# Optimization experiments

Measured on AMD Instinct MI355X. Metric: run time of the kernel, lower is better.

The kernel has to match this reference:

```python
import jax, jax.numpy as jnp
import numpy as np
import math

V, D = 100000, 128
B, L = 4096, 200
INIT_MU = 0.1
INIT_RHO = math.log(math.exp(0.01 ** 0.5) - 1.0)  # softplus^-1(sqrt(init_sigma2))


def setup_inputs() -> dict:
    key = jax.random.key(0)
    k_mu, k_eps, k_x = jax.random.split(key, 3)
    W_mu = jax.random.uniform(k_mu, (V, D), jnp.float32, -INIT_MU, INIT_MU)
    W_rho = jnp.full((V, D), INIT_RHO, dtype=jnp.float32)
    eps = jax.random.normal(k_eps, (V, D), jnp.float32)
    x = jax.random.randint(k_x, (B, L), 0, V)
    return {"x": x, "W_mu": W_mu, "W_rho": W_rho, "eps": eps}


def reference(x, W_mu, W_rho, eps):
    # sigma = softplus(rho); sampled table = mu + sigma * clip(eps, -10, 10)
    W_sigma = jnp.log1p(jnp.exp(W_rho))
    sampled = W_mu + W_sigma * jnp.clip(eps, -10.0, 10.0)  # [V, D]
    return jnp.take(sampled, x, axis=0)  # [B, L, D]
```

## Files before the change

kernel.cpp:

```cpp
#include <hip/hip_runtime.h>
#include <hip/hip_bf16.h>

typedef float f32x4 __attribute__((ext_vector_type(4)));

#define D4 32

__device__ __forceinline__ float softplus_f(float r) {
    return (r > 20.0f) ? r : log1pf(__expf(r));
}
__device__ __forceinline__ float clip10(float e) {
    return fminf(fmaxf(e, -10.0f), 10.0f);
}

__global__ __launch_bounds__(256) void sample_table_kernel(
    const f32x4* __restrict__ mu,
    const f32x4* __restrict__ rho,
    const f32x4* __restrict__ eps,
    f32x4* __restrict__ sampled,
    long n4)
{
    long i = (long)blockIdx.x * blockDim.x + threadIdx.x;
    if (i >= n4) return;
    f32x4 m = __builtin_nontemporal_load(&mu[i]);
    f32x4 r = __builtin_nontemporal_load(&rho[i]);
    f32x4 e = __builtin_nontemporal_load(&eps[i]);
    f32x4 o;
    o.x = m.x + softplus_f(r.x) * clip10(e.x);
    o.y = m.y + softplus_f(r.y) * clip10(e.y);
    o.z = m.z + softplus_f(r.z) * clip10(e.z);
    o.w = m.w + softplus_f(r.w) * clip10(e.w);
    sampled[i] = o;
}

__global__ __launch_bounds__(256) void gather_kernel(
    const int* __restrict__ x,
    const f32x4* __restrict__ sampled,
    f32x4* __restrict__ out,
    int n_rows)
{
    int tid  = blockIdx.x * blockDim.x + threadIdx.x;
    int row  = tid >> 5;
    int lane = tid & 31;
    if (row >= n_rows) return;
    int v = x[row];
    f32x4 val = sampled[(long)v * D4 + lane];
    __builtin_nontemporal_store(val, &out[(long)row * D4 + lane]);
}

__global__ __launch_bounds__(256) void fused_kernel(
    const int* __restrict__ x,
    const f32x4* __restrict__ mu,
    const f32x4* __restrict__ rho,
    const f32x4* __restrict__ eps,
    f32x4* __restrict__ out,
    int n_rows)
{
    int tid  = blockIdx.x * blockDim.x + threadIdx.x;
    int row  = tid >> 5;
    int lane = tid & 31;
    if (row >= n_rows) return;
    long src = (long)x[row] * D4 + lane;
    f32x4 m = mu[src], r = rho[src], e = eps[src];
    f32x4 o;
    o.x = m.x + softplus_f(r.x) * clip10(e.x);
    o.y = m.y + softplus_f(r.y) * clip10(e.y);
    o.z = m.z + softplus_f(r.z) * clip10(e.z);
    o.w = m.w + softplus_f(r.w) * clip10(e.w);
    out[(long)row * D4 + lane] = o;
}

extern "C" void kernel_launch(void* const* d_in, const int* in_sizes, int n_in,
                              void* d_out, int out_size, void* d_ws, size_t ws_size,
                              hipStream_t stream)
{
    const int*   x   = (const int*)  d_in[0];
    const f32x4* mu  = (const f32x4*)d_in[1];
    const f32x4* rho = (const f32x4*)d_in[2];
    const f32x4* eps = (const f32x4*)d_in[3];
    f32x4* out = (f32x4*)d_out;

    int  n_rows      = in_sizes[0];
    long table_elems = (long)in_sizes[1];
    size_t table_bytes = (size_t)table_elems * sizeof(float);
    const int block = 256;

    if (ws_size >= table_bytes) {
        f32x4* sampled = (f32x4*)d_ws;
        long n4 = table_elems / 4;

        int grid1 = (int)((n4 + block - 1) / block);
        sample_table_kernel<<<grid1, block, 0, stream>>>(mu, rho, eps, sampled, n4);

        long threads2 = (long)n_rows * 32;
        int grid2 = (int)((threads2 + block - 1) / block);
        gather_kernel<<<grid2, block, 0, stream>>>(x, sampled, out, n_rows);
    } else {
        long threads = (long)n_rows * 32;
        int grid = (int)((threads + block - 1) / block);
        fused_kernel<<<grid, block, 0, stream>>>(x, mu, rho, eps, out, n_rows);
    }
}
```

Before: 160.7 us.

## Store sampled embedding table in bf16 and gather two rows per thread

The sampled table is written to the workspace as bf16 instead of fp32, halving its footprint and the bytes written by the sampling pass and read by the gather. The gather kernel expands bf16 back to fp32 and handles two output rows per thread slot. This reduces memory traffic and cache pressure but introduces bf16 rounding error in the output values.

```diff
diff --git a/kernel.cpp b/kernel.cpp
--- a/kernel.cpp
+++ b/kernel.cpp
@@ -2,6 +2,10 @@
 #include <hip/hip_bf16.h>
 
 typedef float f32x4 __attribute__((ext_vector_type(4)));
+typedef unsigned short u16;
+typedef unsigned int   u32;
+typedef u16 u16x4 __attribute__((ext_vector_type(4)));
+typedef u16 u16x8 __attribute__((ext_vector_type(8)));
 
 #define D4 32
 
@@ -11,40 +15,82 @@
 __device__ __forceinline__ float clip10(float e) {
     return fminf(fmaxf(e, -10.0f), 10.0f);
 }
+__device__ __forceinline__ u16 f32_to_bf16_rne(float f) {
+    u32 b = __float_as_uint(f);
+    b += 0x7FFFu + ((b >> 16) & 1u);
+    return (u16)(b >> 16);
+}
+__device__ __forceinline__ float bf16_to_f32(u16 h) {
+    return __uint_as_float(((u32)h) << 16);
+}
 
-__global__ __launch_bounds__(256) void sample_table_kernel(
+__global__ __launch_bounds__(256) void sample_table_bf16_kernel(
     const f32x4* __restrict__ mu,
     const f32x4* __restrict__ rho,
     const f32x4* __restrict__ eps,
-    f32x4* __restrict__ sampled,
+    u16x4* __restrict__ tab,
     long n4)
 {
-    long i = (long)blockIdx.x * blockDim.x + threadIdx.x;
-    if (i >= n4) return;
-    f32x4 m = __builtin_nontemporal_load(&mu[i]);
-    f32x4 r = __builtin_nontemporal_load(&rho[i]);
-    f32x4 e = __builtin_nontemporal_load(&eps[i]);
-    f32x4 o;
-    o.x = m.x + softplus_f(r.x) * clip10(e.x);
-    o.y = m.y + softplus_f(r.y) * clip10(e.y);
-    o.z = m.z + softplus_f(r.z) * clip10(e.z);
-    o.w = m.w + softplus_f(r.w) * clip10(e.w);
-    sampled[i] = o;
+    long t  = (long)blockIdx.x * blockDim.x + threadIdx.x;
+    long j0 = t * 2, j1 = j0 + 1;
+    if (j0 >= n4) return;
+
+    f32x4 m0 = __builtin_nontemporal_load(&mu[j0]);
+    f32x4 r0 = __builtin_nontemporal_load(&rho[j0]);
+    f32x4 e0 = __builtin_nontemporal_load(&eps[j0]);
+
+    u16x4 o0;
+    o0.x = f32_to_bf16_rne(m0.x + softplus_f(r0.x) * clip10(e0.x));
+    o0.y = f32_to_bf16_rne(m0.y + softplus_f(r0.y) * clip10(e0.y));
+    o0.z = f32_to_bf16_rne(m0.z + softplus_f(r0.z) * clip10(e0.z));
+    o0.w = f32_to_bf16_rne(m0.w + softplus_f(r0.w) * clip10(e0.w));
+
+    if (j1 < n4) {
+        f32x4 m1 = __builtin_nontemporal_load(&mu[j1]);
+        f32x4 r1 = __builtin_nontemporal_load(&rho[j1]);
+        f32x4 e1 = __builtin_nontemporal_load(&eps[j1]);
+        u16x8 o;
+        o[0] = o0.x; o[1] = o0.y; o[2] = o0.z; o[3] = o0.w;
+        o[4] = f32_to_bf16_rne(m1.x + softplus_f(r1.x) * clip10(e1.x));
+        o[5] = f32_to_bf16_rne(m1.y + softplus_f(r1.y) * clip10(e1.y));
+        o[6] = f32_to_bf16_rne(m1.z + softplus_f(r1.z) * clip10(e1.z));
+        o[7] = f32_to_bf16_rne(m1.w + softplus_f(r1.w) * clip10(e1.w));
+        *(u16x8*)&tab[j0] = o;
+    } else {
+        tab[j0] = o0;
+    }
 }
 
-__global__ __launch_bounds__(256) void gather_kernel(
+__global__ __launch_bounds__(256) void gather_bf16_kernel(
     const int* __restrict__ x,
-    const f32x4* __restrict__ sampled,
+    const u16x4* __restrict__ tab,
     f32x4* __restrict__ out,
-    int n_rows)
+    int n_rows, int S)
 {
-    int tid  = blockIdx.x * blockDim.x + threadIdx.x;
-    int row  = tid >> 5;
-    int lane = tid & 31;
-    if (row >= n_rows) return;
-    int v = x[row];
-    f32x4 val = sampled[(long)v * D4 + lane];
-    __builtin_nontemporal_store(val, &out[(long)row * D4 + lane]);
+    int g    = blockIdx.x * blockDim.x + threadIdx.x;
+    int slot = g >> 5;
+    int lane = g & 31;
+    if (slot >= S) return;
+
+    int r0 = slot, r1 = slot + S;
+    bool h1 = (r1 < n_rows);
+    int v0 = x[r0];
+    int v1 = h1 ? x[r1] : v0;
+
+    u16x4 a = tab[(long)v0 * D4 + lane];
+    u16x4 b = tab[(long)v1 * D4 + lane];
+
+    f32x4 A;
+    A.x = bf16_to_f32(a.x); A.y = bf16_to_f32(a.y);
+    A.z = bf16_to_f32(a.z); A.w = bf16_to_f32(a.w);
+    __builtin_nontemporal_store(A, &out[(long)r0 * D4 + lane]);
+
+    if (h1) {
+        f32x4 B;
+        B.x = bf16_to_f32(b.x); B.y = bf16_to_f32(b.y);
+        B.z = bf16_to_f32(b.z); B.w = bf16_to_f32(b.w);
+        __builtin_nontemporal_store(B, &out[(long)r1 * D4 + lane]);
+    }
 }
 
 __global__ __launch_bounds__(256) void fused_kernel(
@@ -81,19 +127,21 @@
 
     int  n_rows      = in_sizes[0];
     long table_elems = (long)in_sizes[1];
-    size_t table_bytes = (size_t)table_elems * sizeof(float);
+    size_t table_bytes_bf16 = (size_t)table_elems * sizeof(u16);
     const int block = 256;
 
-    if (ws_size >= table_bytes) {
-        f32x4* sampled = (f32x4*)d_ws;
+    if (ws_size >= table_bytes_bf16) {
+        u16x4* tab = (u16x4*)d_ws;
         long n4 = table_elems / 4;
 
-        int grid1 = (int)((n4 + block - 1) / block);
-        sample_table_kernel<<<grid1, block, 0, stream>>>(mu, rho, eps, sampled, n4);
+        long threads1 = (n4 + 1) / 2;
+        int grid1 = (int)((threads1 + block - 1) / block);
+        sample_table_bf16_kernel<<<grid1, block, 0, stream>>>(mu, rho, eps, tab, n4);
 
-        long threads2 = (long)n_rows * 32;
+        int S = (n_rows + 1) / 2;
+        long threads2 = (long)S * 32;
         int grid2 = (int)((threads2 + block - 1) / block);
-        gather_kernel<<<grid2, block, 0, stream>>>(x, sampled, out, n_rows);
+        gather_bf16_kernel<<<grid2, block, 0, stream>>>(x, tab, out, n_rows, S);
     } else {
         long threads = (long)n_rows * 32;
         int grid = (int)((threads + block - 1) / block);
```

Result: faster. 147.2 us (-8.4%).
